# Kernel optimization log

Measured on AMD Instinct MI355X. Metric: run time of the kernel, lower is better.

The kernel has to match this reference:

```python
import jax, jax.numpy as jnp
import numpy as np

# Complete 32-ary tree of depth 3: vocab = 32**3 = 32768 leaves.
B = 4096       # batch
NHID = 512     # hidden size
BR = 32        # branching factor (num_children at every internal node)
DEPTH = 3      # number of internal-node decisions from root to leaf
V = BR ** DEPTH
NUM_NODES = sum(BR ** k for k in range(DEPTH))  # 1 + 32 + 1024 = 1057

# Static tree-indexing tables (level-order node numbering).
_LEVEL_OFFSET = np.array([sum(BR ** j for j in range(k)) for k in range(DEPTH)], dtype=np.int64)   # [0, 1, 33]
_NODE_DIV = np.array([BR ** (DEPTH - k) for k in range(DEPTH)], dtype=np.int64)                    # node-within-level divisor
_STEP_DIV = np.array([BR ** (DEPTH - 1 - k) for k in range(DEPTH)], dtype=np.int64)                # child-step divisor


def setup_inputs() -> dict:
    key = jax.random.key(0)
    k1, k2, k3 = jax.random.split(key, 3)
    inputs = jax.random.normal(k1, (B, NHID), dtype=jnp.float32)
    labels = jax.random.randint(k2, (B,), 0, V)                     # leaf index per sample
    W = jax.random.normal(k3, (NUM_NODES, NHID, BR), dtype=jnp.float32)  # all node params, stacked
    return {"inputs": inputs, "labels": labels, "W": W}


def reference(inputs, labels, W):
    lab = labels[:, None]                                            # [B, 1]
    node_idx = jnp.asarray(_LEVEL_OFFSET)[None, :] + lab // jnp.asarray(_NODE_DIV)[None, :]  # [B, D] node on path
    steps = (lab // jnp.asarray(_STEP_DIV)[None, :]) % BR            # [B, D] child taken at each node
    Wg = W[node_idx]                                                 # [B, D, NHID, BR] gathered path params
    logits = jnp.einsum('bh,bdhc->bdc', inputs, Wg)                  # [B, D, BR]
    p = jax.nn.softmax(logits, axis=-1)
    step_p = jnp.take_along_axis(p, steps[:, :, None], axis=-1)[..., 0]  # [B, D]
    return jnp.prod(step_p, axis=-1)                                 # [B] path probability
```

## Files before the change

kernel.cpp:

```cpp
#include <hip/hip_runtime.h>


#define NHID  512
#define BR    32
#define BATCH 4096
#define NBUCK 1024

__global__ __launch_bounds__(1024) void k_sort(const int* __restrict__ labels,
                                               int* __restrict__ order) {
    __shared__ int labs[BATCH];
    __shared__ int hist[NBUCK];
    __shared__ int scn[NBUCK];
    const int t = threadIdx.x;

    hist[t] = 0;
    #pragma unroll
    for (int r = 0; r < BATCH / 1024; ++r)
        labs[t + 1024 * r] = labels[t + 1024 * r];
    __syncthreads();
    #pragma unroll
    for (int r = 0; r < BATCH / 1024; ++r)
        atomicAdd(&hist[labs[t + 1024 * r] >> 5], 1);
    __syncthreads();

    const int cnt = hist[t];
    scn[t] = cnt;
    __syncthreads();
    for (int d = 1; d < NBUCK; d <<= 1) {
        int u = (t >= d) ? scn[t - d] : 0;
        __syncthreads();
        scn[t] += u;
        __syncthreads();
    }
    hist[t] = scn[t] - cnt;
    __syncthreads();

    #pragma unroll
    for (int r = 0; r < BATCH / 1024; ++r) {
        int j = t + 1024 * r;
        int pos = atomicAdd(&hist[labs[j] >> 5], 1);
        order[pos] = j;
    }
}

__global__ __launch_bounds__(192) void hsm_kernel(
    const float* __restrict__ inputs,
    const int* __restrict__ labels,
    const float* __restrict__ W,
    const int* __restrict__ order,
    float* __restrict__ out)
{
    __shared__ float xs[NHID];
    __shared__ float pk[3];

    const int bidx = blockIdx.x;
    const int r  = (bidx & 7) * (BATCH / 8) + (bidx >> 3);
    const int b  = order[r];
    const int tid = threadIdx.x;

    if (tid < NHID / 4) {
        ((float4*)xs)[tid] = ((const float4*)(inputs + (size_t)b * NHID))[tid];
    }
    __syncthreads();

    const int k    = tid >> 6;
    const int lane = tid & 63;
    const int lab  = labels[b];

    int node, step;
    if (k == 0)      { node = 0;                 step = (lab >> 10) & 31; }
    else if (k == 1) { node = 1 + (lab >> 10);   step = (lab >> 5)  & 31; }
    else             { node = 33 + (lab >> 5);   step = lab & 31;         }

    const int colg  = lane & 7;
    const int hbase = lane >> 3;
    const float4* wp = (const float4*)(W + (size_t)node * (NHID * BR) + hbase * BR + colg * 4);

    float a0 = 0.f, a1 = 0.f, a2 = 0.f, a3 = 0.f;
    #pragma unroll 8
    for (int i = 0; i < NHID / 8; ++i) {
        float4 w = wp[i * (8 * BR / 4)];
        float  x = xs[hbase + 8 * i];
        a0 = fmaf(x, w.x, a0);
        a1 = fmaf(x, w.y, a1);
        a2 = fmaf(x, w.z, a2);
        a3 = fmaf(x, w.w, a3);
    }

    for (int m = 8; m <= 32; m <<= 1) {
        a0 += __shfl_xor(a0, m);
        a1 += __shfl_xor(a1, m);
        a2 += __shfl_xor(a2, m);
        a3 += __shfl_xor(a3, m);
    }

    float mx = fmaxf(fmaxf(a0, a1), fmaxf(a2, a3));
    for (int m = 1; m <= 4; m <<= 1) mx = fmaxf(mx, __shfl_xor(mx, m));
    float es = expf(a0 - mx) + expf(a1 - mx) + expf(a2 - mx) + expf(a3 - mx);
    for (int m = 1; m <= 4; m <<= 1) es += __shfl_xor(es, m);

    const int e = step & 3;
    float v = (e == 0) ? a0 : (e == 1) ? a1 : (e == 2) ? a2 : a3;
    float sl = __shfl(v, step >> 2);
    float p = expf(sl - mx) / es;

    if (lane == 0) pk[k] = p;
    __syncthreads();
    if (tid == 0) out[b] = pk[0] * pk[1] * pk[2];
}

extern "C" void kernel_launch(void* const* d_in, const int* in_sizes, int n_in,
                              void* d_out, int out_size, void* d_ws, size_t ws_size,
                              hipStream_t stream)
{
    const float* inputs = (const float*)d_in[0];
    const int*   labels = (const int*)d_in[1];
    const float* W      = (const float*)d_in[2];
    float* out = (float*)d_out;
    int* order = (int*)d_ws;

    k_sort    <<<dim3(1),     dim3(1024), 0, stream>>>(labels, order);
    hsm_kernel<<<dim3(BATCH), dim3(192),  0, stream>>>(inputs, labels, W, order, out);
}
```

Baseline: 132.4 us.

## Group samples sharing a level-2 node so each block reuses W tiles across four samples

The sort kernel now also emits group descriptors that split each bucket of samples sharing the same level-1/level-2 path into groups of up to four. The compute kernel processes one group per block, loading each W float4 once and applying it to four transposed input vectors held in shared memory. This divides W traffic by up to four. In exchange, blocks are launched at a fixed upper bound and exit early past the group count, and per-thread register use rises.

```diff
diff --git a/kernel.cpp b/kernel.cpp
--- a/kernel.cpp
+++ b/kernel.cpp
@@ -5,12 +5,23 @@
 #define BR    32
 #define BATCH 4096
 #define NBUCK 1024
+#define SMAX  4
+#define GMAX  2048
+
+#define FMA4(A, xv, wv_) do { \
+    (A).x = fmaf((xv), (wv_).x, (A).x); \
+    (A).y = fmaf((xv), (wv_).y, (A).y); \
+    (A).z = fmaf((xv), (wv_).z, (A).z); \
+    (A).w = fmaf((xv), (wv_).w, (A).w); } while (0)
 
 __global__ __launch_bounds__(1024) void k_sort(const int* __restrict__ labels,
-                                               int* __restrict__ order) {
+                                               int* __restrict__ order,
+                                               int* __restrict__ ngroups,
+                                               int* __restrict__ gdesc) {
     __shared__ int labs[BATCH];
     __shared__ int hist[NBUCK];
     __shared__ int scn[NBUCK];
+    __shared__ int gsc[NBUCK];
     const int t = threadIdx.x;
 
     hist[t] = 0;
@@ -23,16 +34,28 @@
         atomicAdd(&hist[labs[t + 1024 * r] >> 5], 1);
     __syncthreads();
 
-    const int cnt = hist[t];
+    const int cnt  = hist[t];
+    const int gcnt = (cnt + SMAX - 1) / SMAX;
     scn[t] = cnt;
+    gsc[t] = gcnt;
     __syncthreads();
     for (int d = 1; d < NBUCK; d <<= 1) {
-        int u = (t >= d) ? scn[t - d] : 0;
+        int u1 = (t >= d) ? scn[t - d] : 0;
+        int u2 = (t >= d) ? gsc[t - d] : 0;
         __syncthreads();
-        scn[t] += u;
+        scn[t] += u1;
+        gsc[t] += u2;
         __syncthreads();
     }
-    hist[t] = scn[t] - cnt;
+    const int off  = scn[t] - cnt;
+    const int goff = gsc[t] - gcnt;
+    hist[t] = off;
+
+    for (int j = 0; j < gcnt; ++j)
+        gdesc[goff + j] = (off + j * SMAX)
+                        | (min(SMAX, cnt - j * SMAX) << 12)
+                        | (t << 16);
+    if (t == NBUCK - 1) *ngroups = gsc[t];
     __syncthreads();
 
     #pragma unroll
@@ -43,70 +66,104 @@
     }
 }
 
-__global__ __launch_bounds__(192) void hsm_kernel(
+__global__ __launch_bounds__(192) void hsm_g4(
     const float* __restrict__ inputs,
     const int* __restrict__ labels,
     const float* __restrict__ W,
     const int* __restrict__ order,
+    const int* __restrict__ ngroups,
+    const int* __restrict__ gdesc,
     float* __restrict__ out)
 {
-    __shared__ float xs[NHID];
-    __shared__ float pk[3];
+    __shared__ float xsT[NHID * SMAX];
+    __shared__ float pk[3][SMAX];
+    __shared__ int   sids[SMAX];
+    __shared__ int   slab[SMAX];
 
-    const int bidx = blockIdx.x;
-    const int r  = (bidx & 7) * (BATCH / 8) + (bidx >> 3);
-    const int b  = order[r];
-    const int tid = threadIdx.x;
+    const int gid = blockIdx.x;
+    if (gid >= *ngroups) return;
+    const int d     = gdesc[gid];
+    const int start = d & 0xFFF;
+    const int m     = (d >> 12) & 0xF;
+    const int g     = d >> 16;
+    const int tid   = threadIdx.x;
 
-    if (tid < NHID / 4) {
-        ((float4*)xs)[tid] = ((const float4*)(inputs + (size_t)b * NHID))[tid];
+    if (tid < SMAX) {
+        int sid = (tid < m) ? order[start + tid] : -1;
+        sids[tid] = sid;
+        slab[tid] = (sid >= 0) ? labels[sid] : 0;
+    }
+    __syncthreads();
+
+    for (int h = tid; h < NHID; h += 192) {
+        float v[SMAX];
+        #pragma unroll
+        for (int s = 0; s < SMAX; ++s) {
+            int id = sids[s];
+            v[s] = (id >= 0) ? inputs[(size_t)id * NHID + h] : 0.0f;
+        }
+        ((float4*)xsT)[h] = make_float4(v[0], v[1], v[2], v[3]);
     }
     __syncthreads();
 
     const int k    = tid >> 6;
     const int lane = tid & 63;
-    const int lab  = labels[b];
+    const int colg = lane & 7;
+    const int hsel = lane >> 3;
 
-    int node, step;
-    if (k == 0)      { node = 0;                 step = (lab >> 10) & 31; }
-    else if (k == 1) { node = 1 + (lab >> 10);   step = (lab >> 5)  & 31; }
-    else             { node = 33 + (lab >> 5);   step = lab & 31;         }
+    const int node = (k == 0) ? 0 : (k == 1) ? 1 + (g >> 5) : 33 + g;
+    const int step01 = (k == 0) ? (g >> 5) : (g & 31);
 
-    const int colg  = lane & 7;
-    const int hbase = lane >> 3;
-    const float4* wp = (const float4*)(W + (size_t)node * (NHID * BR) + hbase * BR + colg * 4);
+    const float4* wp = (const float4*)(W + (size_t)node * (NHID * BR))
+                       + hsel * 8 + colg;
+    const float4* xp = (const float4*)xsT + hsel;
 
-    float a0 = 0.f, a1 = 0.f, a2 = 0.f, a3 = 0.f;
+    float4 acc[SMAX];
+    #pragma unroll
+    for (int s = 0; s < SMAX; ++s) acc[s] = make_float4(0, 0, 0, 0);
+
     #pragma unroll 8
-    for (int i = 0; i < NHID / 8; ++i) {
-        float4 w = wp[i * (8 * BR / 4)];
-        float  x = xs[hbase + 8 * i];
-        a0 = fmaf(x, w.x, a0);
-        a1 = fmaf(x, w.y, a1);
-        a2 = fmaf(x, w.z, a2);
-        a3 = fmaf(x, w.w, a3);
+    for (int i = 0; i < 64; ++i) {
+        float4 w  = wp[i * 64];
+        float4 x4 = xp[i * 8];
+        FMA4(acc[0], x4.x, w);
+        FMA4(acc[1], x4.y, w);
+        FMA4(acc[2], x4.z, w);
+        FMA4(acc[3], x4.w, w);
     }
 
-    for (int m = 8; m <= 32; m <<= 1) {
-        a0 += __shfl_xor(a0, m);
-        a1 += __shfl_xor(a1, m);
-        a2 += __shfl_xor(a2, m);
-        a3 += __shfl_xor(a3, m);
+    #pragma unroll
+    for (int s = 0; s < SMAX; ++s) {
+        #pragma unroll
+        for (int mm = 8; mm <= 32; mm <<= 1) {
+            acc[s].x += __shfl_xor(acc[s].x, mm);
+            acc[s].y += __shfl_xor(acc[s].y, mm);
+            acc[s].z += __shfl_xor(acc[s].z, mm);
+            acc[s].w += __shfl_xor(acc[s].w, mm);
+        }
     }
 
-    float mx = fmaxf(fmaxf(a0, a1), fmaxf(a2, a3));
-    for (int m = 1; m <= 4; m <<= 1) mx = fmaxf(mx, __shfl_xor(mx, m));
-    float es = expf(a0 - mx) + expf(a1 - mx) + expf(a2 - mx) + expf(a3 - mx);
-    for (int m = 1; m <= 4; m <<= 1) es += __shfl_xor(es, m);
+    #pragma unroll
+    for (int s = 0; s < SMAX; ++s) {
+        float4 a = acc[s];
+        float mx = fmaxf(fmaxf(a.x, a.y), fmaxf(a.z, a.w));
+        #pragma unroll
+        for (int mm = 1; mm <= 4; mm <<= 1) mx = fmaxf(mx, __shfl_xor(mx, mm));
+        float es = expf(a.x - mx) + expf(a.y - mx) + expf(a.z - mx) + expf(a.w - mx);
+        #pragma unroll
+        for (int mm = 1; mm <= 4; mm <<= 1) es += __shfl_xor(es, mm);
 
-    const int e = step & 3;
-    float v = (e == 0) ? a0 : (e == 1) ? a1 : (e == 2) ? a2 : a3;
-    float sl = __shfl(v, step >> 2);
-    float p = expf(sl - mx) / es;
+        int step = (k == 2) ? (slab[s] & 31) : step01;
+        int e = step & 3;
+        float v = (e == 0) ? a.x : (e == 1) ? a.y : (e == 2) ? a.z : a.w;
+        float sl = __shfl(v, step >> 2);
+        float p = expf(sl - mx) / es;
+        if (lane == 0) pk[k][s] = p;
+    }
+    __syncthreads();
 
-    if (lane == 0) pk[k] = p;
-    __syncthreads();
-    if (tid == 0) out[b] = pk[0] * pk[1] * pk[2];
+    if (tid < SMAX && sids[tid] >= 0)
+        out[sids[tid]] = pk[0][tid] * pk[1][tid] * pk[2][tid];
 }
 
 extern "C" void kernel_launch(void* const* d_in, const int* in_sizes, int n_in,
@@ -117,8 +174,13 @@
     const int*   labels = (const int*)d_in[1];
     const float* W      = (const float*)d_in[2];
     float* out = (float*)d_out;
-    int* order = (int*)d_ws;
 
-    k_sort    <<<dim3(1),     dim3(1024), 0, stream>>>(labels, order);
-    hsm_kernel<<<dim3(BATCH), dim3(192),  0, stream>>>(inputs, labels, W, order, out);
+    char* ws = (char*)d_ws;
+    int* order   = (int*)ws;
+    int* ngroups = (int*)(ws + 16384);
+    int* gdesc   = (int*)(ws + 16384 + 128);
+
+    k_sort<<<dim3(1),    dim3(1024), 0, stream>>>(labels, order, ngroups, gdesc);
+    hsm_g4<<<dim3(GMAX), dim3(192),  0, stream>>>(inputs, labels, W, order,
+                                                  ngroups, gdesc, out);
 }
```

Result: faster. 122.7 us (-7.3%).
